# Kernel optimization log

Measured on AMD Instinct MI355X. Metric: run time of the kernel, lower is better.

The kernel has to match this reference:

```python
import jax, jax.numpy as jnp
import numpy as np

ALPHA = 0.25  # sparsity init kwarg


def setup_inputs() -> dict:
    key = jax.random.key(0)
    x = jax.random.uniform(key, (32, 256, 256, 16), dtype=jnp.float32)
    return {"x": x}


def reference(x):
    # Original TF code loops over every pixel i in H*W, slicing (B,1,C) and
    # calling force_sparsity, where p = reduce_mean over the WHOLE slice
    # (batch AND channel). Vectorized: p has shape (H, W).
    p = jnp.mean(x, axis=(0, 3))            # (H, W) per-pixel mean over B,C
    p_b = p[None, :, :, None]                # broadcast to (1, H, W, 1)
    beta = (1.0 - ALPHA) / (1.0 - p_b)
    le = p_b >= ALPHA                        # branch selector per pixel
    out = jnp.where(le,
                    x * ALPHA / p_b,
                    1.0 - beta * (1.0 - x))
    return out
```

## Files before the change

### kernel.cpp

```cpp
#include <hip/hip_runtime.h>


#define ALPHA 0.25f

typedef float v4f __attribute__((ext_vector_type(4)));

__global__ __launch_bounds__(256) void rescale_prob_mask_kernel(
    const float* __restrict__ x, float* __restrict__ out) {
  constexpr long F4_PER_B = 256L * 256 * 16 / 4;

  __shared__ float4 stage[8][256];
  __shared__ float lds[4][16];

  const int tile = blockIdx.x;
  const int h    = tile >> 4;
  const int w0   = (tile & 15) << 4;
  const long tile_base_f4 = (((long)h * 256 + w0) * 16) >> 2;

  const int t    = threadIdx.x;
  const int lane = t & 63;
  const int wv   = t >> 6;

  const float4* __restrict__ p4 =
      (const float4*)x + tile_base_f4 + (long)wv * F4_PER_B + lane;
  float* __restrict__ obase =
      (float*)out + 4 * (tile_base_f4 + (long)wv * F4_PER_B + lane);

  float s = 0.0f;
#pragma unroll
  for (int k = 0; k < 8; ++k) {
    float4 v = p4[(long)k * 4 * F4_PER_B];
    stage[k][t] = v;
    s += (v.x + v.y) + (v.z + v.w);
  }

  s += __shfl_xor(s, 1);
  s += __shfl_xor(s, 2);

  const int wp = lane >> 2;
  if ((lane & 3) == 0) lds[wv][wp] = s;
  __syncthreads();
  const float psum = (lds[0][wp] + lds[1][wp]) + (lds[2][wp] + lds[3][wp]);
  const float p = psum * (1.0f / 512.0f);

  float a, d;
  if (p >= ALPHA) {
    a = ALPHA / p;
    d = 0.0f;
  } else {
    const float beta = (1.0f - ALPHA) / (1.0f - p);
    a = beta;
    d = 1.0f - beta;
  }

#pragma unroll
  for (int k = 0; k < 8; ++k) {
    float4 v = stage[k][t];
    v4f r;
    r.x = fmaf(a, v.x, d);
    r.y = fmaf(a, v.y, d);
    r.z = fmaf(a, v.z, d);
    r.w = fmaf(a, v.w, d);
    __builtin_nontemporal_store(
        r, (v4f*)(obase + (long)k * 4 * F4_PER_B * 4));
  }
}

extern "C" void kernel_launch(void* const* d_in, const int* in_sizes, int n_in,
                              void* d_out, int out_size, void* d_ws, size_t ws_size,
                              hipStream_t stream) {
  const float* x = (const float*)d_in[0];
  float* out = (float*)d_out;
  rescale_prob_mask_kernel<<<dim3(4096), dim3(256), 0, stream>>>(x, out);
}
```

Baseline: 242.0 us.

## Split fused reduce-apply into zero, atomic reduce, and streaming apply kernels

Replaces the single fused kernel, which staged each pixel tile's batch slices in LDS, with three kernels. The first zeroes a workspace, the second reads contiguous rows and accumulates per-pixel sums with atomics, and the third re-reads x and applies the affine rescale with fast reciprocals. The aim is fully contiguous, coalesced accesses instead of strided per-batch gathers. The cost is reading the input twice (about 134MB extra traffic), atomic contention, and two extra launches. The reciprocal approximation may also change precision slightly.

```diff
diff --git a/kernel.cpp b/kernel.cpp
--- a/kernel.cpp
+++ b/kernel.cpp
@@ -1,68 +1,72 @@
 #include <hip/hip_runtime.h>
 
 
+typedef float v4f __attribute__((ext_vector_type(4)));
+
 #define ALPHA 0.25f
 
-typedef float v4f __attribute__((ext_vector_type(4)));
+__global__ __launch_bounds__(256) void zero_p(float* __restrict__ p) {
+  p[blockIdx.x * 256 + threadIdx.x] = 0.0f;
+}
 
-__global__ __launch_bounds__(256) void rescale_prob_mask_kernel(
-    const float* __restrict__ x, float* __restrict__ out) {
-  constexpr long F4_PER_B = 256L * 256 * 16 / 4;
+__global__ __launch_bounds__(256) void reduce_p(const float* __restrict__ x,
+                                                float* __restrict__ p) {
+  const int r = blockIdx.x;
+  const int t = threadIdx.x;
+  const float4* __restrict__ row = (const float4*)x + (long)r * 1024;
 
-  __shared__ float4 stage[8][256];
-  __shared__ float lds[4][16];
+  float4 v[4];
+#pragma unroll
+  for (int j = 0; j < 4; ++j) v[j] = row[t + 256 * j];
 
-  const int tile = blockIdx.x;
-  const int h    = tile >> 4;
-  const int w0   = (tile & 15) << 4;
-  const long tile_base_f4 = (((long)h * 256 + w0) * 16) >> 2;
+  float s[4];
+#pragma unroll
+  for (int j = 0; j < 4; ++j) s[j] = (v[j].x + v[j].y) + (v[j].z + v[j].w);
 
-  const int t    = threadIdx.x;
-  const int lane = t & 63;
-  const int wv   = t >> 6;
-
-  const float4* __restrict__ p4 =
-      (const float4*)x + tile_base_f4 + (long)wv * F4_PER_B + lane;
-  float* __restrict__ obase =
-      (float*)out + 4 * (tile_base_f4 + (long)wv * F4_PER_B + lane);
-
-  float s = 0.0f;
 #pragma unroll
-  for (int k = 0; k < 8; ++k) {
-    float4 v = p4[(long)k * 4 * F4_PER_B];
-    stage[k][t] = v;
-    s += (v.x + v.y) + (v.z + v.w);
+  for (int j = 0; j < 4; ++j) {
+    s[j] += __shfl_xor(s[j], 1);
+    s[j] += __shfl_xor(s[j], 2);
   }
 
-  s += __shfl_xor(s, 1);
-  s += __shfl_xor(s, 2);
+  const int h = r & 255;
+  if ((t & 3) == 0) {
+    const int wbase = t >> 2;
+#pragma unroll
+    for (int j = 0; j < 4; ++j)
+      atomicAdd(&p[h * 256 + wbase + 64 * j], s[j]);
+  }
+}
 
-  const int wp = lane >> 2;
-  if ((lane & 3) == 0) lds[wv][wp] = s;
-  __syncthreads();
-  const float psum = (lds[0][wp] + lds[1][wp]) + (lds[2][wp] + lds[3][wp]);
-  const float p = psum * (1.0f / 512.0f);
-
-  float a, d;
-  if (p >= ALPHA) {
-    a = ALPHA / p;
-    d = 0.0f;
-  } else {
-    const float beta = (1.0f - ALPHA) / (1.0f - p);
-    a = beta;
-    d = 1.0f - beta;
-  }
+__global__ __launch_bounds__(256) void apply_k(const float* __restrict__ x,
+                                               const float* __restrict__ p,
+                                               float* __restrict__ out) {
+  constexpr long STRIDE = 8192L * 256;
+  const long i0 = (long)blockIdx.x * 256 + threadIdx.x;
 
 #pragma unroll
-  for (int k = 0; k < 8; ++k) {
-    float4 v = stage[k][t];
+  for (int it = 0; it < 4; ++it) {
+    const long i = i0 + (long)it * STRIDE;
+    float4 v = ((const float4*)x)[i];
+    const int hw = (int)((i >> 2) & 65535);
+    const float pv = p[hw] * (1.0f / 512.0f);
+
+    float a, d;
+    if (pv >= ALPHA) {
+      a = ALPHA * __builtin_amdgcn_rcpf(pv);
+      d = 0.0f;
+    } else {
+      const float beta = (1.0f - ALPHA) * __builtin_amdgcn_rcpf(1.0f - pv);
+      a = beta;
+      d = 1.0f - beta;
+    }
+
     v4f r;
     r.x = fmaf(a, v.x, d);
     r.y = fmaf(a, v.y, d);
     r.z = fmaf(a, v.z, d);
     r.w = fmaf(a, v.w, d);
-    __builtin_nontemporal_store(
-        r, (v4f*)(obase + (long)k * 4 * F4_PER_B * 4));
+    __builtin_nontemporal_store(r, (v4f*)out + i);
   }
 }
 
@@ -71,5 +75,9 @@
                               hipStream_t stream) {
   const float* x = (const float*)d_in[0];
   float* out = (float*)d_out;
-  rescale_prob_mask_kernel<<<dim3(4096), dim3(256), 0, stream>>>(x, out);
+  float* p = (float*)d_ws;
+
+  zero_p<<<dim3(256), dim3(256), 0, stream>>>(p);
+  reduce_p<<<dim3(8192), dim3(256), 0, stream>>>(x, p);
+  apply_k<<<dim3(8192), dim3(256), 0, stream>>>(x, p, out);
 }
```

Measured after the change: 245.3 us. Within noise of the previous version (+1.4%).
